# Optimization experiments

Measured on AMD Instinct MI355X. Metric: run time of the kernel, lower is better.

The kernel has to match this reference:

```python
import jax, jax.numpy as jnp
import numpy as np

NF = 64
DG = 8
NB = 5
K = 3
K2 = K * K


def conv2d(x, w, b):
    # x: [B,C,H,W], w: [O,I,3,3] -> SAME padding, stride 1
    y = jax.lax.conv_general_dilated(x, w, (1, 1), 'SAME',
                                     dimension_numbers=('NCHW', 'OIHW', 'NCHW'))
    return y + b[None, :, None, None]


def dcn(x, off_feat, cw, cb, w, b):
    """Modulated deformable conv (DCNv2, extra_offset_mask=True).
    x: [B,C,H,W] sampled input; off_feat: [B,C,H,W] feeds conv_offset_mask.
    cw/cb: offset-mask conv params [3*DG*K2, C, 3, 3]; w/b: main conv [O, C, 3, 3].
    """
    B, C, H, W = x.shape
    Cg = C // DG
    om = conv2d(off_feat, cw, cb)                      # [B, 3*DG*K2, H, W]
    o1, o2, m = jnp.split(om, 3, axis=1)
    dy = o1.reshape(B, DG, K2, H, W)
    dx = o2.reshape(B, DG, K2, H, W)
    mask = jax.nn.sigmoid(m).reshape(B, DG, K2, H, W)
    # kernel tap offsets for 3x3, pad=1, dilation=1
    kyy, kxx = np.meshgrid(np.arange(K) - 1, np.arange(K) - 1, indexing='ij')
    ky = jnp.asarray(kyy.reshape(K2), x.dtype)
    kx = jnp.asarray(kxx.reshape(K2), x.dtype)
    gy = jnp.arange(H, dtype=x.dtype)
    gx = jnp.arange(W, dtype=x.dtype)
    py = gy[None, None, None, :, None] + ky[None, None, :, None, None] + dy  # [B,DG,K2,H,W]
    px = gx[None, None, None, None, :] + kx[None, None, :, None, None] + dx
    y0 = jnp.floor(py)
    x0 = jnp.floor(px)
    wy = py - y0
    wx = px - x0
    y0i = y0.astype(jnp.int32)
    x0i = x0.astype(jnp.int32)
    xg = x.reshape(B, DG, Cg, H * W)

    def gather(iy, ix):
        valid = ((iy >= 0) & (iy < H) & (ix >= 0) & (ix < W)).astype(x.dtype)
        lin = (jnp.clip(iy, 0, H - 1) * W + jnp.clip(ix, 0, W - 1)).reshape(B, DG, 1, K2 * H * W)
        v = jnp.take_along_axis(xg, jnp.broadcast_to(lin, (B, DG, Cg, K2 * H * W)), axis=3)
        return v.reshape(B, DG, Cg, K2, H, W) * valid[:, :, None]

    v00 = gather(y0i, x0i)
    v01 = gather(y0i, x0i + 1)
    v10 = gather(y0i + 1, x0i)
    v11 = gather(y0i + 1, x0i + 1)
    wy_ = wy[:, :, None]
    wx_ = wx[:, :, None]
    val = (v00 * (1 - wy_) * (1 - wx_) + v01 * (1 - wy_) * wx_
           + v10 * wy_ * (1 - wx_) + v11 * wy_ * wx_) * mask[:, :, None]  # [B,DG,Cg,K2,H,W]
    wr = w.reshape(w.shape[0], DG, Cg, K2)
    out = jnp.einsum('bgckhw,ogck->bohw', val, wr) + b[None, :, None, None]
    return out


def setup_inputs() -> dict:
    key = jax.random.key(0)
    ks = jax.random.split(key, 16)

    def w_(k, shape, s=0.05):
        return jax.random.normal(k, shape, jnp.float32) * s

    B, N, C, H, W = 4, 5, 1, 128, 128
    inp = {}
    inp['x'] = jax.random.normal(ks[0], (B, N, C, H, W), jnp.float32)
    inp['w_init'] = w_(ks[1], (NF, C, 3, 3))
    inp['b_init'] = jnp.zeros((NF,), jnp.float32)
    inp['res_w1'] = w_(ks[2], (NB, NF, NF, 3, 3))
    inp['res_b1'] = jnp.zeros((NB, NF), jnp.float32)
    inp['res_w2'] = w_(ks[3], (NB, NF, NF, 3, 3))
    inp['res_b2'] = jnp.zeros((NB, NF), jnp.float32)
    inp['w_bn'] = w_(ks[4], (NF, 2 * NF, 3, 3))
    inp['b_bn'] = jnp.zeros((NF,), jnp.float32)
    inp['off_w'] = w_(ks[5], (4, NF, NF, 3, 3))
    inp['off_b'] = jnp.zeros((4, NF), jnp.float32)
    inp['com_w'] = w_(ks[6], (4, 3 * DG * K2, NF, 3, 3), 0.01)
    inp['com_b'] = jnp.zeros((4, 3 * DG * K2), jnp.float32)
    inp['dcn_w'] = w_(ks[7], (4, NF, NF, 3, 3))
    inp['dcn_b'] = jnp.zeros((4, NF), jnp.float32)
    inp['w_rec'] = w_(ks[8], (C, NF, 3, 3))
    inp['b_rec'] = jnp.zeros((C,), jnp.float32)
    return inp


def reference(x, w_init, b_init, res_w1, res_b1, res_w2, res_b2, w_bn, b_bn,
              off_w, off_b, com_w, com_b, dcn_w, dcn_b, w_rec, b_rec):
    B, N, C, H, W = x.shape
    y = x.reshape(B * N, C, H, W)
    out = jax.nn.relu(conv2d(y, w_init, b_init))
    for i in range(NB):  # ResidualBlock_noBN x nb
        h = jax.nn.relu(conv2d(out, res_w1[i], res_b1[i]))
        out = out + conv2d(h, res_w2[i], res_b2[i])
    out = out.reshape(B, N, NF, H, W)
    ref = out[:, N // 2]
    ys = []
    for i in range(N):
        nei = out[:, i]
        fea = conv2d(jnp.concatenate([ref, nei], axis=1), w_bn, b_bn)
        o = conv2d(fea, off_w[0], off_b[0])
        fea = dcn(fea, o, com_w[0], com_b[0], dcn_w[0], dcn_b[0])
        o = conv2d(fea, off_w[1], off_b[1])
        fea = dcn(fea, o, com_w[1], com_b[1], dcn_w[1], dcn_b[1])
        o = conv2d(fea, off_w[2], off_b[2])
        fea = dcn(nei, o, com_w[2], com_b[2], dcn_w[2], dcn_b[2])
        o = conv2d(fea, off_w[3], off_b[3])
        aligned = dcn(fea, o, com_w[3], com_b[3], dcn_w[3], dcn_b[3])
        ys.append(conv2d(aligned, w_rec, b_rec))
    return jnp.concatenate(ys, axis=1)  # [B, N*C, H, W]
```

## Files before the change

kernel.cpp:

```cpp
#include <hip/hip_runtime.h>
#include <hip/hip_bf16.h>

typedef __hip_bfloat16 bf16;
typedef __attribute__((ext_vector_type(8))) short short8;
typedef __attribute__((ext_vector_type(4))) float floatx4;
typedef unsigned short ush;

#define HH 128
#define WW 128
#define HW 16384

__device__ __forceinline__ float b2f(bf16 v){ return __bfloat162float(v); }
__device__ __forceinline__ float bfu2f(ush u){
  union{unsigned int i; float f;} c; c.i = ((unsigned int)u)<<16; return c.f;
}
__device__ __forceinline__ ush f2bfu(float f){
  bf16 h = __float2bfloat16(f);
  return *(ush*)&h;
}

__global__ void detect_dtype(const ush* __restrict__ x, float* __restrict__ flag){
  __shared__ int bad;
  if (threadIdx.x==0) bad = 0;
  __syncthreads();
  for (int j=threadIdx.x; j<4096; j+=256){
    float f = bfu2f(x[j]);
    if (!(fabsf(f) < 1e4f)) atomicOr(&bad, 1);
  }
  __syncthreads();
  if (threadIdx.x==0) flag[0] = bad ? 0.f : 1.f;
}

struct CvtArgs { const void* src[17]; int dst[17]; };
__global__ void convert_all(CvtArgs a, float* __restrict__ ws, const float* __restrict__ flag){
  static const int N[17] = {327680, 576, 64, 184320, 320, 184320, 320,
                            73728, 64, 147456, 256, 497664, 864, 147456,
                            256, 576, 1};
  int i = blockIdx.y;
  int idx = blockIdx.x*256 + threadIdx.x;
  if (idx >= N[i]) return;
  float v = (flag[0] > 0.5f) ? b2f(((const bf16*)a.src[i])[idx])
                             : ((const float*)a.src[i])[idx];
  ws[a.dst[i] + idx] = v;
}

__global__ void transpose_w(const float* __restrict__ src, float* __restrict__ dst, int Co, int CiK){
  int tid = blockIdx.x*256 + threadIdx.x;
  if (tid >= Co*CiK) return;
  int co = tid / CiK, r = tid - co*CiK;
  dst[(long)r*Co + co] = src[tid];
}

struct PackArgs { int src[20]; int dst[20]; short Cout[20]; short Cin[20];
                  short kh[20]; short nOcB[20]; };
__global__ void pack_all(PackArgs a, const float* __restrict__ ws, ush* __restrict__ wsu){
  int jb = blockIdx.y;
  int idx = blockIdx.x*256 + threadIdx.x;
  int nOcB = a.nOcB[jb];
  int total = nOcB*36864;
  if (idx >= total) return;
  const float* src = ws + a.src[jb];
  ush* dst = wsu + 2*(size_t)a.dst[jb];
  int Cout = a.Cout[jb], Cin = a.Cin[jb], kh = a.kh[jb];
  int ocb = idx / 36864; int r = idx - ocb*36864;
  int c  = r & 7;
  int lx = (r>>3) & 15;
  int n  = (r>>7) & 3;
  int lk = (r>>9) & 3;
  int j  = r>>11;
  int t = j>>1, ch = j&1;
  int oc = n*16+lx;
  int k = ch*32 + lk*8 + c;
  int ocg = ocb*64 + oc, icg = kh*64 + k;
  float v = (ocg < Cout && icg < Cin) ? src[((long)ocg*Cin + icg)*9 + t] : 0.f;
  dst[idx] = f2bfu(v);
}

__global__ void pack_dcn_w(const float* __restrict__ src0, ush* __restrict__ dst0){
  int s = blockIdx.y;
  const float* src = src0 + (long)s*36864;
  ush* dst = dst0 + (long)s*49152;
  int idx = blockIdx.x*256 + threadIdx.x;
  if (idx >= 49152) return;
  int g = idx / 6144; int r = idx - g*6144;
  int oc = r / 96; int k = r - oc*96;
  float v = 0.f;
  if (k < 72){
    int tap = k >> 3, c = k & 7;
    v = src[((long)oc*64 + g*8 + c)*9 + tap];
  }
  dst[idx] = f2bfu(v);
}

__global__ __launch_bounds__(256) void conv_init_kernel(const float* __restrict__ x,
    const float* __restrict__ wT, const float* __restrict__ bias,
    ush* __restrict__ fh, ush* __restrict__ fl){
  __shared__ ush L[256*66];
  int tid = threadIdx.x;
  int tx = tid & 15, ty = tid >> 4;
  int gx = blockIdx.x*16+tx, gy = blockIdx.y*16+ty;
  int n = blockIdx.z;
  const float* xp = x + (long)n*HW;
  float v[9];
  #pragma unroll
  for (int dy=0;dy<3;dy++)
    #pragma unroll
    for (int dx=0;dx<3;dx++){
      int yy = gy+dy-1, xx = gx+dx-1;
      bool ok = (yy>=0)&&(yy<HH)&&(xx>=0)&&(xx<WW);
      v[dy*3+dx] = ok ? xp[yy*WW+xx] : 0.f;
    }
  float acc[64];
  #pragma unroll 1
  for (int oc=0; oc<64; oc++){
    float a = bias[oc];
    #pragma unroll
    for (int k=0;k<9;k++) a = fmaf(v[k], wT[k*64+oc], a);
    acc[oc] = fmaxf(a, 0.f);
  }
  #pragma unroll 1
  for (int pass=0; pass<2; pass++){
    #pragma unroll 1
    for (int oc=0; oc<64; oc++){
      float a = acc[oc];
      ush h = f2bfu(a);
      L[tid*66+oc] = pass ? f2bfu(a - bfu2f(h)) : h;
    }
    __syncthreads();
    ush* dst = pass ? fl : fh;
    for (int j=tid; j<2048; j+=256){
      int c8 = j&7, pidx = j>>3;
      int row = pidx>>4, col = pidx&15;
      long addr = ((long)n*HW + (blockIdx.y*16+row)*WW + blockIdx.x*16+col)*64 + c8*8;
      *(short8*)(dst+addr) = *(const short8*)(L + pidx*66 + c8*8);
    }
    __syncthreads();
  }
}

template<int NPL, int MINW, int MT>
__global__ __launch_bounds__(256, MINW) void conv_mfma(
    const ush* __restrict__ in_hi, const ush* __restrict__ in_lo, long in_ps,
    const ush* __restrict__ in2_hi, const ush* __restrict__ in2_lo, long in2_ps,
    const ush* __restrict__ wpack, const ush* __restrict__ wpack2,
    const float* __restrict__ bias, int has_bias,
    const ush* __restrict__ add_hi, const ush* __restrict__ add_lo,
    long add_ps, int add_cs,
    ush* __restrict__ out_hi, ush* __restrict__ out_lo,
    long out_ps, int out_cs,
    ush* __restrict__ out_pb, int pf_C,
    ush* __restrict__ gp_out,
    int Cout, int nOcB, int relu)
{
  constexpr int ROWS = 4*MT + 2;
  constexpr int APX  = ROWS*18;
  constexpr int NPX  = 4*MT*16;
  constexpr int LDSN = (NPL*APX*64 > 2*NPX*66) ? NPL*APX*64 : 2*NPX*66;
  __shared__ ush A[LDSN];
  int tid = threadIdx.x;
  int z = blockIdx.z; int img = z / nOcB; int ocb = z - img*nOcB;
  int x0 = blockIdx.x*16 - 1, y0 = blockIdx.y*(4*MT) - 1;
  int w = tid>>6, l = tid&63, lx = l&15, lk = l>>4;
  floatx4 acc[MT][4];
  #pragma unroll
  for (int mt=0;mt<MT;mt++)
    #pragma unroll
    for (int n=0;n<4;n++) acc[mt][n] = (floatx4){0.f,0.f,0.f,0.f};

  auto phase = [&](const ush* ihb, const ush* ilb, const ush* wfb){
    __syncthreads();
    #pragma unroll
    for (int p=0;p<NPL;p++){
      const ush* src = p ? ilb : ihb;
      ush* dstp = A + p*APX*64;
      for (int j=tid; j<APX*8; j+=256){
        int pidx = j>>3, c8 = j&7;
        int row = pidx/18, col = pidx - row*18;
        int yy = y0+row, xx = x0+col;
        uint4 v = make_uint4(0u,0u,0u,0u);
        if ((unsigned)yy < 128u && (unsigned)xx < 128u)
          v = *(const uint4*)(src + ((long)(yy*WW+xx))*64 + c8*8);
        *(uint4*)(dstp + pidx*64 + ((c8 ^ (pidx&7))<<3)) = v;
      }
    }
    const ush* wfrag = wfb + lk*4*128 + lx*8;
    short8 bf[4][4];
    #pragma unroll
    for (int s=0;s<3;s++)
      #pragma unroll
      for (int n=0;n<4;n++)
        bf[s][n] = *(const short8*)(wfrag + (s*16 + n)*128);
    __syncthreads();
    #pragma unroll
    for (int j=0;j<18;j++){
      int t = j>>1, ch = j&1;
      if (j<15){
        #pragma unroll
        for (int n=0;n<4;n++)
          bf[(j+3)&3][n] = *(const short8*)(wfrag + ((j+3)*16 + n)*128);
      }
      int ky = t/3, kx = t - ky*3;
      int jc = ch*4 + lk;
      #pragma unroll
      for (int mt=0; mt<MT; mt++){
        int pidx = (w*MT+mt+ky)*18 + lx + kx;
        #pragma unroll
        for (int p=0;p<NPL;p++){
          short8 af = *(const short8*)(A + p*APX*64 + pidx*64 + ((jc ^ (pidx&7))<<3));
          #pragma unroll
          for (int n=0;n<4;n++)
            acc[mt][n] = __builtin_amdgcn_mfma_f32_16x16x32_bf16(af, bf[j&3][n], acc[mt][n], 0,0,0);
        }
      }
    }
  };
  phase(in_hi + (long)img*in_ps*64, in_lo + (long)img*in_ps*64,
        wpack + (long)ocb*36864);
  if (wpack2)
    phase(in2_hi + (long)img*in2_ps*64, in2_lo + (long)img*in2_ps*64,
          wpack2 + (long)ocb*36864);

  int ybase = blockIdx.y*(4*MT) + w*MT;
  int xbase = blockIdx.x*16 + lk*4;
  if (out_pb){
    #pragma unroll
    for (int mt=0;mt<MT;mt++){
      int y = ybase + mt;
      #pragma unroll
      for (int n=0;n<4;n++){
        int ocg = ocb*64 + n*16 + lx;
        if (ocg < Cout){
          float bv = has_bias ? bias[ocg] : 0.f;
          #pragma unroll
          for (int r=0;r<4;r++){
            int xg = xbase + r;
            out_pb[((long)img*pf_C + ocg)*HW + y*WW + xg] = f2bfu(acc[mt][n][r] + bv);
          }
        }
      }
    }
  } else {
    __syncthreads();
    ush* L0 = A;
    ush* L1 = A + NPX*66;
    #pragma unroll
    for (int mt=0;mt<MT;mt++){
      int y = ybase + mt;
      int rowl = w*MT + mt;
      #pragma unroll
      for (int n=0;n<4;n++){
        int ocg = n*16 + lx;
        float bv = has_bias ? bias[ocg] : 0.f;
        #pragma unroll
        for (int r=0;r<4;r++){
          int coll = lk*4 + r;
          float v = acc[mt][n][r] + bv;
          if (add_hi){
            long ap = ((long)img*add_ps + y*WW + blockIdx.x*16 + coll)*add_cs + ocg;
            v += bfu2f(add_hi[ap]) + bfu2f(add_lo[ap]);
          }
          if (relu) v = fmaxf(v, 0.f);
          ush h = f2bfu(v);
          L0[(rowl*16+coll)*66 + ocg] = h;
          if (out_lo) L1[(rowl*16+coll)*66 + ocg] = f2bfu(v - bfu2f(h));
        }
      }
    }
    __syncthreads();
    for (int j=tid; j<NPX*8; j+=256){
      int pidx = j>>3, c8 = j&7;
      int row = pidx>>4, col = pidx&15;
      long pix = (blockIdx.y*(4*MT)+row)*WW + blockIdx.x*16+col;
      long pp = (long)img*out_ps + pix;
      short8 h8 = *(const short8*)(L0 + pidx*66 + c8*8);
      *(short8*)(out_hi + pp*64 + c8*8) = h8;
      if (out_lo){
        short8 l8 = *(const short8*)(L1 + pidx*66 + c8*8);
        *(short8*)(out_lo + pp*64 + c8*8) = l8;
        if (gp_out){
          short8 g;
          #pragma unroll
          for (int c=0;c<8;c++)
            g[c] = (short)f2bfu(bfu2f((ush)h8[c]) + bfu2f((ush)l8[c]));
          *(short8*)(gp_out + (((long)(img*8+c8))*HW + pix)*8) = g;
        }
      }
    }
  }
}

__global__ __launch_bounds__(256,4) void res_fused(
    const ush* __restrict__ src_h, const ush* __restrict__ src_l,
    const ush* __restrict__ w1, const float* __restrict__ b1,
    const ush* __restrict__ w2, const float* __restrict__ b2,
    ush* __restrict__ dst_h, ush* __restrict__ dst_l)
{
  __shared__ ush F[180*64];
  __shared__ ush Hs[112*64];
  int tid = threadIdx.x;
  int bx = blockIdx.x, by = blockIdx.y, img = blockIdx.z;
  int fy0 = by*4 - 2, fx0 = bx*16 - 2;
  int w = tid>>6, l = tid&63, lx = l&15, lk = l>>4;
  const ush* sh = src_h + (long)img*HW*64;
  for (int j=tid; j<1440; j+=256){
    int pidx = j>>3, c8 = j&7;
    int row = pidx/20, col = pidx - row*20;
    int yy = fy0+row, xx = fx0+col;
    uint4 v = make_uint4(0u,0u,0u,0u);
    if ((unsigned)yy<128u && (unsigned)xx<128u)
      v = *(const uint4*)(sh + ((long)(yy*WW+xx))*64 + c8*8);
    *(uint4*)(F + pidx*64 + ((c8 ^ (pidx&7))<<3)) = v;
  }
  const ush* wf1 = w1 + lk*4*128 + lx*8;
  int hrow[2], hcol[2], hvalid[2];
  #pragma unroll
  for (int mm=0;mm<2;mm++){
    int m = w + mm*4;
    hvalid[mm] = (m < 7);
    int hp = m*16 + lx;
    hrow[mm] = hp/18; hcol[mm] = hp - hrow[mm]*18;
  }
  floatx4 acc1[2][4];
  #pragma unroll
  for (int mm=0;mm<2;mm++)
    #pragma unroll
    for (int n=0;n<4;n++) acc1[mm][n] = (floatx4){0.f,0.f,0.f,0.f};
  short8 bf[4][4];
  #pragma unroll
  for (int s=0;s<3;s++)
    #pragma unroll
    for (int n=0;n<4;n++)
      bf[s][n] = *(const short8*)(wf1 + (s*16 + n)*128);
  __syncthreads();
  #pragma unroll
  for (int j=0;j<18;j++){
    int t = j>>1, ch = j&1;
    if (j<15){
      #pragma unroll
      for (int n=0;n<4;n++)
        bf[(j+3)&3][n] = *(const short8*)(wf1 + ((j+3)*16 + n)*128);
    }
    int ky = t/3, kx = t - ky*3;
    int jc = ch*4 + lk;
    #pragma unroll
    for (int mm=0;mm<2;mm++){
      if (!hvalid[mm]) continue;
      int pidx = (hrow[mm]+ky)*20 + hcol[mm] + kx;
      short8 af = *(const short8*)(F + pidx*64 + ((jc ^ (pidx&7))<<3));
      #pragma unroll
      for (int n=0;n<4;n++)
        acc1[mm][n] = __builtin_amdgcn_mfma_f32_16x16x32_bf16(af, bf[j&3][n], acc1[mm][n], 0,0,0);
    }
  }
  #pragma unroll
  for (int mm=0;mm<2;mm++){
    if (!hvalid[mm]) continue;
    int m = w + mm*4;
    #pragma unroll
    for (int n=0;n<4;n++){
      int oc = n*16+lx;
      float bv = b1[oc];
      #pragma unroll
      for (int r=0;r<4;r++){
        int hp = m*16 + lk*4 + r;
        int hr = hp/18, hc = hp - hr*18;
        int fy = fy0 + 1 + hr, fx = fx0 + 1 + hc;
        bool inimg = ((unsigned)fy < 128u) && ((unsigned)fx < 128u);
        float v = inimg ? fmaxf(acc1[mm][n][r] + bv, 0.f) : 0.f;
        Hs[hp*64 + (((oc>>3) ^ (hp&7))<<3) + (oc&7)] = f2bfu(v);
      }
    }
  }
  __syncthreads();
  const ush* wf2 = w2 + lk*4*128 + lx*8;
  floatx4 acc2[4];
  #pragma unroll
  for (int n=0;n<4;n++) acc2[n] = (floatx4){0.f,0.f,0.f,0.f};
  #pragma unroll
  for (int s=0;s<3;s++)
    #pragma unroll
    for (int n=0;n<4;n++)
      bf[s][n] = *(const short8*)(wf2 + (s*16 + n)*128);
  #pragma unroll
  for (int j=0;j<18;j++){
    int t = j>>1, ch = j&1;
    if (j<15){
      #pragma unroll
      for (int n=0;n<4;n++)
        bf[(j+3)&3][n] = *(const short8*)(wf2 + ((j+3)*16 + n)*128);
    }
    int ky = t/3, kx = t - ky*3;
    int jc = ch*4 + lk;
    int pidx = (w+ky)*18 + lx + kx;
    short8 af = *(const short8*)(Hs + pidx*64 + ((jc ^ (pidx&7))<<3));
    #pragma unroll
    for (int n=0;n<4;n++)
      acc2[n] = __builtin_amdgcn_mfma_f32_16x16x32_bf16(af, bf[j&3][n], acc2[n], 0,0,0);
  }
  const ush* sl = src_l + (long)img*HW*64;
  int gy = by*4 + w;
  float vout[4][4];
  #pragma unroll
  for (int n=0;n<4;n++){
    int oc = n*16+lx;
    float bv = b2[oc];
    #pragma unroll
    for (int r=0;r<4;r++){
      int colp = lk*4 + r;
      int gx = bx*16 + colp;
      int pt = (w+2)*20 + colp + 2;
      float fh = bfu2f(F[pt*64 + (((oc>>3) ^ (pt&7))<<3) + (oc&7)]);
      float fl = bfu2f(sl[((long)(gy*WW+gx))*64 + oc]);
      vout[n][r] = acc2[n][r] + bv + fh + fl;
    }
  }
  __syncthreads();
  ush* L0 = F;
  ush* L1 = F + 64*66;
  #pragma unroll
  for (int n=0;n<4;n++){
    int oc = n*16+lx;
    #pragma unroll
    for (int r=0;r<4;r++){
      int px = w*16 + lk*4 + r;
      float v = vout[n][r];
      ush h = f2bfu(v);
      L0[px*66 + oc] = h;
      L1[px*66 + oc] = f2bfu(v - bfu2f(h));
    }
  }
  __syncthreads();
  for (int j=tid; j<512; j+=256){
    int pidx = j>>3, c8 = j&7;
    int row = pidx>>4, col = pidx&15;
    long pp = ((long)img*HW + (by*4+row)*WW + bx*16+col)*64 + c8*8;
    *(short8*)(dst_h + pp) = *(const short8*)(L0 + pidx*66 + c8*8);
    *(short8*)(dst_l + pp) = *(const short8*)(L1 + pidx*66 + c8*8);
  }
}

__global__ __launch_bounds__(256) void repack_gp(const ush* __restrict__ in_h,
    const ush* __restrict__ in_l, long in_ps, ush* __restrict__ gp){
  long idx = (long)blockIdx.x*256 + threadIdx.x;
  int img = (int)(idx >> 17);
  int rem = (int)(idx & 131071);
  int pix = rem >> 3, c8 = rem & 7;
  long src = ((long)img*in_ps + pix)*64 + c8*8;
  short8 h = *(const short8*)(in_h+src);
  short8 lo = *(const short8*)(in_l+src);
  short8 o;
  #pragma unroll
  for (int c=0;c<8;c++) o[c] = (short)f2bfu(bfu2f((ush)h[c]) + bfu2f((ush)lo[c]));
  *(short8*)(gp + (((long)(img*8+c8))*HW + pix)*8) = o;
}

__global__ __launch_bounds__(256) void dcn_mfma(
    const ush* __restrict__ gp,
    const ush* __restrict__ om,
    const ush* __restrict__ wpk,
    const float* __restrict__ bias,
    ush* __restrict__ out_hi, ush* __restrict__ out_lo,
    ush* __restrict__ gp_out)
{
  __shared__ ush S[13312];
  ush* Ah = S;
  ush* Bt = S + 6656;
  int tid = threadIdx.x;
  int half = blockIdx.x, gy = blockIdx.y, img = blockIdx.z;
  int xoff = half*64;
  {
    short8 z = {0,0,0,0,0,0,0,0};
    for (int j=tid; j<192; j+=256){
      int px = j/3, c = j - px*3;
      *(short8*)(Ah + px*104 + 72 + c*8) = z;
    }
  }
  int w = tid>>6, l = tid&63, lx = l&15, lk = l>>4;
  int px_s = tid & 63, q = tid >> 6;
  int t0 = (q==0)?0:(q*2+1), t1 = t0 + ((q==0)?3:2);
  const ush* omb = om + (long)img*216*HW + gy*WW + xoff + px_s;
  floatx4 acc[4];
  #pragma unroll
  for (int n=0;n<4;n++) acc[n] = (floatx4){0.f,0.f,0.f,0.f};

  #pragma unroll 1
  for (int g=0; g<8; g++){
    __syncthreads();
    const ush* wsrc = wpk + g*6144;
    for (int j=tid; j<768; j+=256){
      int oc = j/12, kc = j - oc*12;
      *(short8*)(Bt + oc*104 + kc*8) = *(const short8*)(wsrc + oc*96 + kc*8);
    }
    const ush* gpb = gp + ((long)(img*8+g))*HW*8;
    #pragma unroll 1
    for (int t=t0; t<t1; t++){
      int ch = g*9+t;
      float dy = bfu2f(omb[(long)ch*HW]);
      float dx = bfu2f(omb[(long)(72+ch)*HW]);
      float mv = bfu2f(omb[(long)(144+ch)*HW]);
      float m = 1.f/(1.f+__expf(-mv));
      float py = (float)gy + (float)(t/3 - 1) + dy;
      float pxf = (float)(xoff + px_s) + (float)(t%3 - 1) + dx;
      float fy = floorf(py), fx = floorf(pxf);
      int y0 = (int)fy, x0 = (int)fx;
      float wy = py - fy, wx = pxf - fx;
      bool y0v = (y0>=0 && y0<HH), y1v = (y0+1>=0 && y0+1<HH);
      bool x0v = (x0>=0 && x0<WW), x1v = (x0+1>=0 && x0+1<WW);
      float w00 = (1.f-wy)*(1.f-wx)*m * ((y0v&&x0v)?1.f:0.f);
      float w01 = (1.f-wy)*wx*m      * ((y0v&&x1v)?1.f:0.f);
      float w10 = wy*(1.f-wx)*m      * ((y1v&&x0v)?1.f:0.f);
      float w11 = wy*wx*m            * ((y1v&&x1v)?1.f:0.f);
      int y0c = min(max(y0,0),HH-1), y1c = min(max(y0+1,0),HH-1);
      int x0c = min(max(x0,0),WW-1), x1c = min(max(x0+1,0),WW-1);
      short8 s00 = *(const short8*)(gpb + (((long)(y0c*WW+x0c))<<3));
      short8 s01 = *(const short8*)(gpb + (((long)(y0c*WW+x1c))<<3));
      short8 s10 = *(const short8*)(gpb + (((long)(y1c*WW+x0c))<<3));
      short8 s11 = *(const short8*)(gpb + (((long)(y1c*WW+x1c))<<3));
      short8 vh;
      #pragma unroll
      for (int c=0;c<8;c++){
        float val = w00*bfu2f((ush)s00[c]) + w01*bfu2f((ush)s01[c])
                  + w10*bfu2f((ush)s10[c]) + w11*bfu2f((ush)s11[c]);
        vh[c] = (short)f2bfu(val);
      }
      *(short8*)(Ah + px_s*104 + t*8) = vh;
    }
    __syncthreads();
    #pragma unroll
    for (int ks=0; ks<3; ks++){
      short8 bfg[4];
      #pragma unroll
      for (int n=0;n<4;n++)
        bfg[n] = *(const short8*)(Bt + (n*16+lx)*104 + ks*32 + lk*8);
      int px = w*16 + lx;
      short8 ah = *(const short8*)(Ah + px*104 + ks*32 + lk*8);
      #pragma unroll
      for (int n=0;n<4;n++)
        acc[n] = __builtin_amdgcn_mfma_f32_16x16x32_bf16(ah, bfg[n], acc[n], 0,0,0);
    }
  }
  __syncthreads();
  ush* L0 = S;
  ush* L1 = S + 64*66;
  #pragma unroll
  for (int n=0;n<4;n++){
    int oc = n*16 + lx;
    float bv = bias[oc];
    #pragma unroll
    for (int r=0;r<4;r++){
      int pxl = w*16 + lk*4 + r;
      float v = acc[n][r] + bv;
      ush h = f2bfu(v);
      L0[pxl*66 + oc] = h;
      L1[pxl*66 + oc] = f2bfu(v - bfu2f(h));
    }
  }
  __syncthreads();
  long base = ((long)img*HW + gy*WW + xoff)*64;
  for (int j=tid; j<512; j+=256){
    int pidx = j>>3, c8 = j&7;
    short8 h8 = *(const short8*)(L0 + pidx*66 + c8*8);
    short8 l8 = *(const short8*)(L1 + pidx*66 + c8*8);
    *(short8*)(out_hi + base + pidx*64 + c8*8) = h8;
    *(short8*)(out_lo + base + pidx*64 + c8*8) = l8;
    if (gp_out){
      short8 g8;
      #pragma unroll
      for (int c=0;c<8;c++)
        g8[c] = (short)f2bfu(bfu2f((ush)h8[c]) + bfu2f((ush)l8[c]));
      *(short8*)(gp_out + (((long)(img*8+c8))*HW + gy*WW + xoff + pidx)*8) = g8;
    }
  }
}

__global__ __launch_bounds__(256) void rec_kernel(
    const ush* __restrict__ fh, const ush* __restrict__ fl,
    const float* __restrict__ wT, const float* __restrict__ bias,
    void* __restrict__ out, int ni, const float* __restrict__ flag){
  __shared__ float red[256];
  int tid = threadIdx.x;
  int p = tid & 31, q = tid >> 5;
  int gx = blockIdx.x*32 + p;
  int gy = blockIdx.y;
  int b = blockIdx.z;
  float acc = 0.f;
  #pragma unroll
  for (int t=0;t<9;t++){
    int yy = gy + t/3 - 1, xx = gx + t%3 - 1;
    if (yy<0||yy>=HH||xx<0||xx>=WW) continue;
    long base = ((long)b*HW + yy*WW + xx)*64 + q*8;
    short8 h = *(const short8*)(fh + base);
    short8 lo = *(const short8*)(fl + base);
    #pragma unroll
    for (int cc=0;cc<8;cc++){
      float v = bfu2f((ush)h[cc]) + bfu2f((ush)lo[cc]);
      acc = fmaf(v, wT[(q*8+cc)*9 + t], acc);
    }
  }
  red[q*32+p] = acc;
  __syncthreads();
  if (tid < 32){
    float s = bias[0];
    #pragma unroll
    for (int k=0;k<8;k++) s += red[k*32+tid];
    long idx = ((long)b*5+ni)*HW + gy*WW + blockIdx.x*32 + tid;
    if (flag[0] > 0.5f) ((bf16*)out)[idx] = __float2bfloat16(s);
    else                ((float*)out)[idx] = s;
  }
}

extern "C" void kernel_launch(void* const* d_in, const int* in_sizes, int n_in,
                              void* d_out, int out_size, void* d_ws, size_t ws_size,
                              hipStream_t stream) {
  float* ws = (float*)d_ws;

  size_t off = 16;
  auto alloc = [&](size_t nel){ size_t o = off; off += (nel + 7) & ~(size_t)7; return o; };

  static const int IN_N[17] = {327680, 576, 64, 184320, 320, 184320, 320,
                               73728, 64, 147456, 256, 497664, 864, 147456,
                               256, 576, 1};
  size_t cin[17];
  for (int i=0;i<17;i++) cin[i] = alloc(IN_N[i]);

  size_t wt_init = alloc(640);
  size_t wdcn_pk[4]; for (int s=0;s<4;s++) wdcn_pk[s] = alloc(24576);
  size_t wt_rec = alloc(640);
  size_t pk_res1[5], pk_res2[5];
  for (int i=0;i<5;i++) pk_res1[i] = alloc(18432);
  for (int i=0;i<5;i++) pk_res2[i] = alloc(18432);
  size_t pk_bn[2]; for (int h=0;h<2;h++) pk_bn[h] = alloc(18432);
  size_t pk_off[4]; for (int s=0;s<4;s++) pk_off[s] = alloc(18432);
  size_t pk_com[4]; for (int s=0;s<4;s++) pk_com[s] = alloc(73728);

  size_t feat_h_o = alloc(10485760);
  size_t feat_l_o = alloc(10485760);
  size_t U = alloc(26738688);

  ush* feat_h = (ush*)(ws + feat_h_o);
  ush* feat_l = (ush*)(ws + feat_l_o);
  ush* alt_h  = (ush*)(ws + U);
  ush* alt_l  = (ush*)(ws + U + 10485760);
  ush* hbuf_h = (ush*)(ws + U + 10485760);
  ush* feaA_h = (ush*)(ws + U);
  ush* feaA_l = (ush*)(ws + U + 2097152);
  ush* feaB_h = (ush*)(ws + U + 4194304);
  ush* feaB_l = (ush*)(ws + U + 6291456);
  ush* obuf_h = (ush*)(ws + U + 8388608);
  ush* gpA    = (ush*)(ws + U + 10485760);
  ush* ombuf  = (ush*)(ws + U + 12582912);
  ush* gpB    = (ush*)(ws + U + 19660800);

  float* flag = ws;

  detect_dtype<<<dim3(1), dim3(256), 0, stream>>>((const ush*)d_in[0], flag);
  {
    CvtArgs ca;
    for (int i=0;i<17;i++){ ca.src[i] = d_in[i]; ca.dst[i] = (int)cin[i]; }
    convert_all<<<dim3(1945,17), dim3(256), 0, stream>>>(ca, ws, flag);
  }
  const float* b_init = ws+cin[2];
  const float* res_b1 = ws+cin[4];
  const float* res_b2 = ws+cin[6];
  const float* b_bn   = ws+cin[8];
  const float* off_b  = ws+cin[10];
  const float* com_b  = ws+cin[12];
  const float* dcn_b  = ws+cin[14];
  const float* b_rec  = ws+cin[16];

  transpose_w<<<dim3(3), dim3(256), 0, stream>>>(ws+cin[1], ws+wt_init, 64, 9);
  transpose_w<<<dim3(3), dim3(256), 0, stream>>>(ws+cin[15], ws+wt_rec, 1, 576);
  pack_dcn_w<<<dim3(192,4), dim3(256), 0, stream>>>(ws+cin[13], (ush*)(ws+wdcn_pk[0]));
  {
    PackArgs pa;
    int j = 0;
    for (int i=0;i<5;i++){ pa.src[j]=(int)(cin[3]+(size_t)i*36864); pa.dst[j]=(int)pk_res1[i];
      pa.Cout[j]=64; pa.Cin[j]=64; pa.kh[j]=0; pa.nOcB[j]=1; j++; }
    for (int i=0;i<5;i++){ pa.src[j]=(int)(cin[5]+(size_t)i*36864); pa.dst[j]=(int)pk_res2[i];
      pa.Cout[j]=64; pa.Cin[j]=64; pa.kh[j]=0; pa.nOcB[j]=1; j++; }
    for (int h=0;h<2;h++){ pa.src[j]=(int)cin[7]; pa.dst[j]=(int)pk_bn[h];
      pa.Cout[j]=64; pa.Cin[j]=128; pa.kh[j]=(short)h; pa.nOcB[j]=1; j++; }
    for (int s=0;s<4;s++){ pa.src[j]=(int)(cin[9]+(size_t)s*36864); pa.dst[j]=(int)pk_off[s];
      pa.Cout[j]=64; pa.Cin[j]=64; pa.kh[j]=0; pa.nOcB[j]=1; j++; }
    for (int s=0;s<4;s++){ pa.src[j]=(int)(cin[11]+(size_t)s*124416); pa.dst[j]=(int)pk_com[s];
      pa.Cout[j]=216; pa.Cin[j]=64; pa.kh[j]=0; pa.nOcB[j]=4; j++; }
    pack_all<<<dim3(576,20), dim3(256), 0, stream>>>(pa, ws, (ush*)ws);
  }

  dim3 cblk(256);
  auto conv = [&](const ush* in_h, const ush* in_l, long in_ps,
                  const ush* in2_h, const ush* in2_l, long in2_ps,
                  size_t pk, const ush* pk2p,
                  const float* bias, int has_bias,
                  const ush* add_h, const ush* add_l, long add_ps, int add_cs,
                  ush* o_h, ush* o_l, long out_ps, int out_cs,
                  ush* o_pb, int pf_C, ush* gp_o,
                  int Cout, int nOcB, int relu, int N, int nPl, int mtMode){
    if (nPl == 2 && mtMode == 2)
      conv_mfma<2,2,2><<<dim3(8,16,N*nOcB), cblk, 0, stream>>>(
          in_h, in_l, in_ps, in2_h, in2_l, in2_ps,
          (const ush*)(ws+pk), pk2p, bias, has_bias,
          add_h, add_l, add_ps, add_cs, o_h, o_l, out_ps, out_cs,
          o_pb, pf_C, gp_o, Cout, nOcB, relu);
    else if (nPl == 2 && mtMode == 1)
      conv_mfma<2,2,1><<<dim3(8,32,N*nOcB), cblk, 0, stream>>>(
          in_h, in_l, in_ps, in2_h, in2_l, in2_ps,
          (const ush*)(ws+pk), pk2p, bias, has_bias,
          add_h, add_l, add_ps, add_cs, o_h, o_l, out_ps, out_cs,
          o_pb, pf_C, gp_o, Cout, nOcB, relu);
    else if (nPl == 1 && mtMode == 1)
      conv_mfma<1,3,1><<<dim3(8,32,N*nOcB), cblk, 0, stream>>>(
          in_h, in_l, in_ps, in2_h, in2_l, in2_ps,
          (const ush*)(ws+pk), pk2p, bias, has_bias,
          add_h, add_l, add_ps, add_cs, o_h, o_l, out_ps, out_cs,
          o_pb, pf_C, gp_o, Cout, nOcB, relu);
    else
      conv_mfma<1,3,2><<<dim3(8,16,N*nOcB), cblk, 0, stream>>>(
          in_h, in_l, in_ps, in2_h, in2_l, in2_ps,
          (const ush*)(ws+pk), pk2p, bias, has_bias,
          add_h, add_l, add_ps, add_cs, o_h, o_l, out_ps, out_cs,
          o_pb, pf_C, gp_o, Cout, nOcB, relu);
  };

  conv_init_kernel<<<dim3(8,8,20), cblk, 0, stream>>>(ws+cin[0], ws+wt_init, b_init,
                                                      feat_h, feat_l);
  conv(feat_h, feat_l, HW, nullptr, nullptr, 0, pk_res1[0], nullptr,
       res_b1, 1,
       nullptr, nullptr, 0, 0, hbuf_h, nullptr, HW, 64, nullptr, 0, nullptr, 64, 1, 1, 20, 2, 1);
  conv(hbuf_h, hbuf_h, HW, nullptr, nullptr, 0, pk_res2[0], nullptr,
       res_b2, 1,
       feat_h, feat_l, HW, 64, feat_h, feat_l, HW, 64, nullptr, 0, nullptr, 64, 1, 0, 20, 1, 1);
  {
    ush *sh = feat_h, *sl = feat_l, *dh = alt_h, *dl = alt_l;
    for (int i=1;i<5;i++){
      res_fused<<<dim3(8,32,20), cblk, 0, stream>>>(
          sh, sl, (const ush*)(ws+pk_res1[i]), res_b1+(size_t)i*64,
          (const ush*)(ws+pk_res2[i]), res_b2+(size_t)i*64, dh, dl);
      ush* t;
      t = sh; sh = dh; dh = t;
      t = sl; sl = dl; dl = t;
    }
  }
  for (int i=0;i<5;i++){
    conv(feat_h + (size_t)2*HW*64, feat_l + (size_t)2*HW*64, 5L*HW,
         feat_h + (size_t)i*HW*64, feat_l + (size_t)i*HW*64, 5L*HW,
         pk_bn[0], (const ush*)(ws+pk_bn[1]), b_bn, 1,
         nullptr, nullptr, 0, 0, feaA_h, feaA_l, HW, 64, nullptr, 0, gpA, 64, 1, 0, 4, 2, 1);
    ush *fa_h = feaA_h, *fa_l = feaA_l, *fb_h = feaB_h, *fb_l = feaB_l;
    for (int s=0;s<4;s++){
      conv(fa_h, fa_h, HW, nullptr, nullptr, 0, pk_off[s], nullptr,
           off_b+(size_t)s*64, 1,
           nullptr, nullptr, 0, 0, obuf_h, nullptr, HW, 64, nullptr, 0, nullptr, 64, 1, 0, 4, 1, 1);
      conv(obuf_h, obuf_h, HW, nullptr, nullptr, 0, pk_com[s], nullptr,
           com_b+(size_t)s*216, 1,
           nullptr, nullptr, 0, 0, nullptr, nullptr, 0, 0, ombuf, 216, nullptr, 216, 4, 0, 4, 1, 2);
      if (s == 2)
        repack_gp<<<dim3(2048), cblk, 0, stream>>>(feat_h + (size_t)i*HW*64,
            feat_l + (size_t)i*HW*64, 5L*HW, gpA);
      const ush* gp_src = (s==0) ? gpA : (s==1) ? gpB : (s==2) ? gpA : gpB;
      ush* gp_dst = (s==0 || s==2) ? gpB : nullptr;
      dcn_mfma<<<dim3(2,128,4), cblk, 0, stream>>>(gp_src, ombuf,
          (const ush*)(ws+wdcn_pk[s]), dcn_b+(size_t)s*64, fb_h, fb_l, gp_dst);
      ush* t;
      t = fa_h; fa_h = fb_h; fb_h = t;
      t = fa_l; fa_l = fb_l; fb_l = t;
    }
    rec_kernel<<<dim3(4,128,4), cblk, 0, stream>>>(fa_h, fa_l, ws+wt_rec, b_rec, d_out, i, flag);
  }
}
```

Measured before the change: 2.931 ms.

## Batch all five neighbor alignment passes into single launches when workspace allows

When the workspace is large enough, the per-neighbor loop over five frames is replaced by one set of launches covering all 20 image-neighbor pairs. The bottleneck, offset, DCN, repack and reconstruction kernels use 5x larger grids with index remapping. The aim is to cut launch count and fill the GPU better, since the old 4-image grids were small. In exchange it needs larger intermediate buffers and keeps the old loop as a fallback for small workspaces.

```diff
diff --git a/kernel.cpp b/kernel.cpp
--- a/kernel.cpp
+++ b/kernel.cpp
@@ -150,7 +150,7 @@
     long out_ps, int out_cs,
     ush* __restrict__ out_pb, int pf_C,
     ush* __restrict__ gp_out,
-    int Cout, int nOcB, int relu)
+    int Cout, int nOcB, int relu, int bnmap)
 {
   constexpr int ROWS = 4*MT + 2;
   constexpr int APX  = ROWS*18;
@@ -214,10 +214,12 @@
       }
     }
   };
-  phase(in_hi + (long)img*in_ps*64, in_lo + (long)img*in_ps*64,
+  long i1 = bnmap ? (long)((img&3)*5 + 2)        : (long)img;
+  long i2 = bnmap ? (long)((img&3)*5 + (img>>2)) : (long)img;
+  phase(in_hi + i1*in_ps*64, in_lo + i1*in_ps*64,
         wpack + (long)ocb*36864);
   if (wpack2)
-    phase(in2_hi + (long)img*in2_ps*64, in2_lo + (long)img*in2_ps*64,
+    phase(in2_hi + i2*in2_ps*64, in2_lo + i2*in2_ps*64,
           wpack2 + (long)ocb*36864);
 
   int ybase = blockIdx.y*(4*MT) + w*MT;
@@ -440,12 +442,13 @@
 }
 
 __global__ __launch_bounds__(256) void repack_gp(const ush* __restrict__ in_h,
-    const ush* __restrict__ in_l, long in_ps, ush* __restrict__ gp){
+    const ush* __restrict__ in_l, long in_ps, ush* __restrict__ gp, int map){
   long idx = (long)blockIdx.x*256 + threadIdx.x;
   int img = (int)(idx >> 17);
   int rem = (int)(idx & 131071);
   int pix = rem >> 3, c8 = rem & 7;
-  long src = ((long)img*in_ps + pix)*64 + c8*8;
+  long isrc = map ? (long)((img&3)*5 + (img>>2)) : (long)img;
+  long src = (isrc*in_ps + pix)*64 + c8*8;
   short8 h = *(const short8*)(in_h+src);
   short8 lo = *(const short8*)(in_l+src);
   short8 o;
@@ -582,13 +585,16 @@
   int p = tid & 31, q = tid >> 5;
   int gx = blockIdx.x*32 + p;
   int gy = blockIdx.y;
-  int b = blockIdx.z;
+  int z = blockIdx.z;
+  int b, slot;
+  if (ni < 0){ b = z & 3; slot = z >> 2; }
+  else       { b = z;     slot = ni;     }
   float acc = 0.f;
   #pragma unroll
   for (int t=0;t<9;t++){
     int yy = gy + t/3 - 1, xx = gx + t%3 - 1;
     if (yy<0||yy>=HH||xx<0||xx>=WW) continue;
-    long base = ((long)b*HW + yy*WW + xx)*64 + q*8;
+    long base = ((long)z*HW + yy*WW + xx)*64 + q*8;
     short8 h = *(const short8*)(fh + base);
     short8 lo = *(const short8*)(fl + base);
     #pragma unroll
@@ -603,7 +609,7 @@
     float s = bias[0];
     #pragma unroll
     for (int k=0;k<8;k++) s += red[k*32+tid];
-    long idx = ((long)b*5+ni)*HW + gy*WW + blockIdx.x*32 + tid;
+    long idx = ((long)b*5+slot)*HW + gy*WW + blockIdx.x*32 + tid;
     if (flag[0] > 0.5f) ((bf16*)out)[idx] = __float2bfloat16(s);
     else                ((float*)out)[idx] = s;
   }
@@ -635,21 +641,37 @@
 
   size_t feat_h_o = alloc(10485760);
   size_t feat_l_o = alloc(10485760);
-  size_t U = alloc(26738688);
+  size_t U = off;
+
+  const size_t PL = 10485760;
+  size_t need_fl = U + 7*PL + 35389440;
+  bool big = ws_size >= need_fl*sizeof(float);
 
   ush* feat_h = (ush*)(ws + feat_h_o);
   ush* feat_l = (ush*)(ws + feat_l_o);
   ush* alt_h  = (ush*)(ws + U);
-  ush* alt_l  = (ush*)(ws + U + 10485760);
-  ush* hbuf_h = (ush*)(ws + U + 10485760);
-  ush* feaA_h = (ush*)(ws + U);
-  ush* feaA_l = (ush*)(ws + U + 2097152);
-  ush* feaB_h = (ush*)(ws + U + 4194304);
-  ush* feaB_l = (ush*)(ws + U + 6291456);
-  ush* obuf_h = (ush*)(ws + U + 8388608);
-  ush* gpA    = (ush*)(ws + U + 10485760);
-  ush* ombuf  = (ush*)(ws + U + 12582912);
-  ush* gpB    = (ush*)(ws + U + 19660800);
+  ush* alt_l  = (ush*)(ws + U + PL);
+  ush* hbuf_h = (ush*)(ws + U + PL);
+  ush *feaA_h, *feaA_l, *feaB_h, *feaB_l, *obuf_h, *gpA, *gpB, *ombuf;
+  if (big){
+    feaA_h = (ush*)(ws + U);
+    feaA_l = (ush*)(ws + U + PL);
+    feaB_h = (ush*)(ws + U + 2*PL);
+    feaB_l = (ush*)(ws + U + 3*PL);
+    obuf_h = (ush*)(ws + U + 4*PL);
+    gpA    = (ush*)(ws + U + 5*PL);
+    gpB    = (ush*)(ws + U + 6*PL);
+    ombuf  = (ush*)(ws + U + 7*PL);
+  } else {
+    feaA_h = (ush*)(ws + U);
+    feaA_l = (ush*)(ws + U + 2097152);
+    feaB_h = (ush*)(ws + U + 4194304);
+    feaB_l = (ush*)(ws + U + 6291456);
+    obuf_h = (ush*)(ws + U + 8388608);
+    gpA    = (ush*)(ws + U + 10485760);
+    ombuf  = (ush*)(ws + U + 12582912);
+    gpB    = (ush*)(ws + U + 19660800);
+  }
 
   float* flag = ws;
 
@@ -695,41 +717,41 @@
                   const ush* add_h, const ush* add_l, long add_ps, int add_cs,
                   ush* o_h, ush* o_l, long out_ps, int out_cs,
                   ush* o_pb, int pf_C, ush* gp_o,
-                  int Cout, int nOcB, int relu, int N, int nPl, int mtMode){
+                  int Cout, int nOcB, int relu, int N, int nPl, int mtMode, int bnmap){
     if (nPl == 2 && mtMode == 2)
       conv_mfma<2,2,2><<<dim3(8,16,N*nOcB), cblk, 0, stream>>>(
           in_h, in_l, in_ps, in2_h, in2_l, in2_ps,
           (const ush*)(ws+pk), pk2p, bias, has_bias,
           add_h, add_l, add_ps, add_cs, o_h, o_l, out_ps, out_cs,
-          o_pb, pf_C, gp_o, Cout, nOcB, relu);
+          o_pb, pf_C, gp_o, Cout, nOcB, relu, bnmap);
     else if (nPl == 2 && mtMode == 1)
       conv_mfma<2,2,1><<<dim3(8,32,N*nOcB), cblk, 0, stream>>>(
           in_h, in_l, in_ps, in2_h, in2_l, in2_ps,
           (const ush*)(ws+pk), pk2p, bias, has_bias,
           add_h, add_l, add_ps, add_cs, o_h, o_l, out_ps, out_cs,
-          o_pb, pf_C, gp_o, Cout, nOcB, relu);
+          o_pb, pf_C, gp_o, Cout, nOcB, relu, bnmap);
     else if (nPl == 1 && mtMode == 1)
       conv_mfma<1,3,1><<<dim3(8,32,N*nOcB), cblk, 0, stream>>>(
           in_h, in_l, in_ps, in2_h, in2_l, in2_ps,
           (const ush*)(ws+pk), pk2p, bias, has_bias,
           add_h, add_l, add_ps, add_cs, o_h, o_l, out_ps, out_cs,
-          o_pb, pf_C, gp_o, Cout, nOcB, relu);
+          o_pb, pf_C, gp_o, Cout, nOcB, relu, bnmap);
     else
       conv_mfma<1,3,2><<<dim3(8,16,N*nOcB), cblk, 0, stream>>>(
           in_h, in_l, in_ps, in2_h, in2_l, in2_ps,
           (const ush*)(ws+pk), pk2p, bias, has_bias,
           add_h, add_l, add_ps, add_cs, o_h, o_l, out_ps, out_cs,
-          o_pb, pf_C, gp_o, Cout, nOcB, relu);
+          o_pb, pf_C, gp_o, Cout, nOcB, relu, bnmap);
   };
 
   conv_init_kernel<<<dim3(8,8,20), cblk, 0, stream>>>(ws+cin[0], ws+wt_init, b_init,
                                                       feat_h, feat_l);
   conv(feat_h, feat_l, HW, nullptr, nullptr, 0, pk_res1[0], nullptr,
        res_b1, 1,
-       nullptr, nullptr, 0, 0, hbuf_h, nullptr, HW, 64, nullptr, 0, nullptr, 64, 1, 1, 20, 2, 1);
+       nullptr, nullptr, 0, 0, hbuf_h, nullptr, HW, 64, nullptr, 0, nullptr, 64, 1, 1, 20, 2, 1, 0);
   conv(hbuf_h, hbuf_h, HW, nullptr, nullptr, 0, pk_res2[0], nullptr,
        res_b2, 1,
-       feat_h, feat_l, HW, 64, feat_h, feat_l, HW, 64, nullptr, 0, nullptr, 64, 1, 0, 20, 1, 1);
+       feat_h, feat_l, HW, 64, feat_h, feat_l, HW, 64, nullptr, 0, nullptr, 64, 1, 0, 20, 1, 1, 0);
   {
     ush *sh = feat_h, *sl = feat_l, *dh = alt_h, *dl = alt_l;
     for (int i=1;i<5;i++){
@@ -741,30 +763,55 @@
       t = sl; sl = dl; dl = t;
     }
   }
-  for (int i=0;i<5;i++){
-    conv(feat_h + (size_t)2*HW*64, feat_l + (size_t)2*HW*64, 5L*HW,
-         feat_h + (size_t)i*HW*64, feat_l + (size_t)i*HW*64, 5L*HW,
+  if (big){
+    conv(feat_h, feat_l, HW, feat_h, feat_l, HW,
          pk_bn[0], (const ush*)(ws+pk_bn[1]), b_bn, 1,
-         nullptr, nullptr, 0, 0, feaA_h, feaA_l, HW, 64, nullptr, 0, gpA, 64, 1, 0, 4, 2, 1);
+         nullptr, nullptr, 0, 0, feaA_h, feaA_l, HW, 64, nullptr, 0, gpA, 64, 1, 0, 20, 2, 1, 1);
     ush *fa_h = feaA_h, *fa_l = feaA_l, *fb_h = feaB_h, *fb_l = feaB_l;
     for (int s=0;s<4;s++){
       conv(fa_h, fa_h, HW, nullptr, nullptr, 0, pk_off[s], nullptr,
            off_b+(size_t)s*64, 1,
-           nullptr, nullptr, 0, 0, obuf_h, nullptr, HW, 64, nullptr, 0, nullptr, 64, 1, 0, 4, 1, 1);
+           nullptr, nullptr, 0, 0, obuf_h, nullptr, HW, 64, nullptr, 0, nullptr, 64, 1, 0, 20, 1, 1, 0);
       conv(obuf_h, obuf_h, HW, nullptr, nullptr, 0, pk_com[s], nullptr,
            com_b+(size_t)s*216, 1,
-           nullptr, nullptr, 0, 0, nullptr, nullptr, 0, 0, ombuf, 216, nullptr, 216, 4, 0, 4, 1, 2);
+           nullptr, nullptr, 0, 0, nullptr, nullptr, 0, 0, ombuf, 216, nullptr, 216, 4, 0, 20, 1, 2, 0);
       if (s == 2)
-        repack_gp<<<dim3(2048), cblk, 0, stream>>>(feat_h + (size_t)i*HW*64,
-            feat_l + (size_t)i*HW*64, 5L*HW, gpA);
+        repack_gp<<<dim3(10240), cblk, 0, stream>>>(feat_h, feat_l, HW, gpA, 1);
       const ush* gp_src = (s==0) ? gpA : (s==1) ? gpB : (s==2) ? gpA : gpB;
       ush* gp_dst = (s==0 || s==2) ? gpB : nullptr;
-      dcn_mfma<<<dim3(2,128,4), cblk, 0, stream>>>(gp_src, ombuf,
+      dcn_mfma<<<dim3(2,128,20), cblk, 0, stream>>>(gp_src, ombuf,
           (const ush*)(ws+wdcn_pk[s]), dcn_b+(size_t)s*64, fb_h, fb_l, gp_dst);
       ush* t;
       t = fa_h; fa_h = fb_h; fb_h = t;
       t = fa_l; fa_l = fb_l; fb_l = t;
     }
-    rec_kernel<<<dim3(4,128,4), cblk, 0, stream>>>(fa_h, fa_l, ws+wt_rec, b_rec, d_out, i, flag);
-  }
-}
+    rec_kernel<<<dim3(4,128,20), cblk, 0, stream>>>(fa_h, fa_l, ws+wt_rec, b_rec, d_out, -1, flag);
+  } else {
+    for (int i=0;i<5;i++){
+      conv(feat_h + (size_t)2*HW*64, feat_l + (size_t)2*HW*64, 5L*HW,
+           feat_h + (size_t)i*HW*64, feat_l + (size_t)i*HW*64, 5L*HW,
+           pk_bn[0], (const ush*)(ws+pk_bn[1]), b_bn, 1,
+           nullptr, nullptr, 0, 0, feaA_h, feaA_l, HW, 64, nullptr, 0, gpA, 64, 1, 0, 4, 2, 1, 0);
+      ush *fa_h = feaA_h, *fa_l = feaA_l, *fb_h = feaB_h, *fb_l = feaB_l;
+      for (int s=0;s<4;s++){
+        conv(fa_h, fa_h, HW, nullptr, nullptr, 0, pk_off[s], nullptr,
+             off_b+(size_t)s*64, 1,
+             nullptr, nullptr, 0, 0, obuf_h, nullptr, HW, 64, nullptr, 0, nullptr, 64, 1, 0, 4, 1, 1, 0);
+        conv(obuf_h, obuf_h, HW, nullptr, nullptr, 0, pk_com[s], nullptr,
+             com_b+(size_t)s*216, 1,
+             nullptr, nullptr, 0, 0, nullptr, nullptr, 0, 0, ombuf, 216, nullptr, 216, 4, 0, 4, 1, 2, 0);
+        if (s == 2)
+          repack_gp<<<dim3(2048), cblk, 0, stream>>>(feat_h + (size_t)i*HW*64,
+              feat_l + (size_t)i*HW*64, 5L*HW, gpA, 0);
+        const ush* gp_src = (s==0) ? gpA : (s==1) ? gpB : (s==2) ? gpA : gpB;
+        ush* gp_dst = (s==0 || s==2) ? gpB : nullptr;
+        dcn_mfma<<<dim3(2,128,4), cblk, 0, stream>>>(gp_src, ombuf,
+            (const ush*)(ws+wdcn_pk[s]), dcn_b+(size_t)s*64, fb_h, fb_l, gp_dst);
+        ush* t;
+        t = fa_h; fa_h = fb_h; fb_h = t;
+        t = fa_l; fa_l = fb_l; fb_l = t;
+      }
+      rec_kernel<<<dim3(4,128,4), cblk, 0, stream>>>(fa_h, fa_l, ws+wt_rec, b_rec, d_out, i, flag);
+    }
+  }
+}
```

After: 2.940 ms. About the same (+0.3%).
